# Performance work log

Hardware: AMD Instinct MI355X
Metric: run time of the kernel (lower is better)

Reference implementation:

```python
import jax, jax.numpy as jnp
import numpy as np

NEG_INF = -9e15
LEAKY_SLOPE = 0.2  # init alpha
N, IN_DIM, OUT_DIM = 8192, 512, 256


def setup_inputs() -> dict:
    key = jax.random.key(0)
    k1, k2, k3, k4, k5 = jax.random.split(key, 5)
    h = jax.random.normal(k1, (N, IN_DIM), dtype=jnp.float32)
    adj = jax.random.randint(k2, (N, N), 0, 2, dtype=jnp.int32)
    W = jax.random.normal(k3, (IN_DIM, OUT_DIM), dtype=jnp.float32) * 0.06
    a_left = jax.random.normal(k4, (OUT_DIM, 1), dtype=jnp.float32) * 0.1
    a_right = jax.random.normal(k5, (OUT_DIM, 1), dtype=jnp.float32) * 0.1
    return {"h": h, "adj": adj, "W": W, "a_left": a_left, "a_right": a_right}


def reference(h, adj, W, a_left, a_right):
    Wh = h @ W                                  # [N, out_dim]
    Wh1 = Wh @ a_left                           # [N, 1]
    Wh2 = Wh @ a_right                          # [N, 1]
    e = Wh1 + Wh2.T                             # [N, N] broadcast additive scores
    e = jnp.where(e > 0, e, LEAKY_SLOPE * e)    # LeakyReLU
    e = jnp.where(adj > 0, e, NEG_INF)          # adjacency mask
    attention = jax.nn.softmax(e, axis=1)       # row-wise softmax (dropout=0, eval)
    h_out = attention @ Wh                      # [N, out_dim]
    return jax.nn.elu(h_out)                    # activation=True
```

## Files before the change

### kernel.cpp

```cpp
#include <hip/hip_runtime.h>
#include <hip/hip_bf16.h>
#include <cstdint>
#include <cstddef>

typedef float  f32x4  __attribute__((ext_vector_type(4)));
typedef __bf16 bf16x8 __attribute__((ext_vector_type(8)));

#define LOG2E 1.4426950408889634f

static constexpr int GN   = 8192;
static constexpr int GIN  = 512;
static constexpr int GOUT = 256;

static __device__ __forceinline__ void gload_lds16(const void* g, void* lds){
  typedef uint32_t __attribute__((address_space(1)))* gp_t;
  typedef uint32_t __attribute__((address_space(3)))* lp_t;
  __builtin_amdgcn_global_load_lds((gp_t)(uintptr_t)g,
                                   (lp_t)(uint32_t)(uintptr_t)lds, 16, 0, 0);
}

__global__ __launch_bounds__(256) void k_pre1(const float* __restrict__ W,
                                              const float* __restrict__ al,
                                              const float* __restrict__ ar,
                                              const float* __restrict__ h,
                                              float* __restrict__ wal,
                                              float* __restrict__ war,
                                              __bf16* __restrict__ WT,
                                              __bf16* __restrict__ hb){
  __shared__ float T[64][65];
  const int bid = blockIdx.x, tid = threadIdx.x;
  if(bid < 128){
    const int k = bid*4 + (tid>>6), lane = tid & 63;
    float4 wv = ((const float4*)(W + (size_t)k*GOUT))[lane];
    float4 av = ((const float4*)al)[lane];
    float4 bv = ((const float4*)ar)[lane];
    float sl = wv.x*av.x + wv.y*av.y + wv.z*av.z + wv.w*av.w;
    float sr = wv.x*bv.x + wv.y*bv.y + wv.z*bv.z + wv.w*bv.w;
    #pragma unroll
    for(int o=32;o;o>>=1){ sl += __shfl_down(sl,o,64); sr += __shfl_down(sr,o,64); }
    if(lane==0){ wal[k] = sl*LOG2E; war[k] = sr*LOG2E; }
  } else if(bid < 160){
    const int tile = bid - 128;
    const int k0 = (tile>>2)*64, c0 = (tile&3)*64;
    const int r = tid>>2, cs = (tid&3)*16;
    #pragma unroll
    for(int j=0;j<4;j++){
      float4 v = *(const float4*)(W + (size_t)(k0+r)*GOUT + c0 + cs + 4*j);
      T[r][cs+4*j+0]=v.x; T[r][cs+4*j+1]=v.y; T[r][cs+4*j+2]=v.z; T[r][cs+4*j+3]=v.w;
    }
    __syncthreads();
    bf16x8 o1, o2;
    #pragma unroll
    for(int j=0;j<8;j++){ o1[j]=(__bf16)T[cs+j][r]; o2[j]=(__bf16)T[cs+8+j][r]; }
    __bf16* dst = WT + (size_t)(c0+r)*GIN + k0 + cs;
    *(bf16x8*)dst = o1;
    *(bf16x8*)(dst+8) = o2;
  } else {
    size_t i = ((size_t)(bid-160)*256 + tid)*8;
    float4 v0 = *(const float4*)(h+i);
    float4 v1 = *(const float4*)(h+i+4);
    bf16x8 o;
    o[0]=(__bf16)v0.x; o[1]=(__bf16)v0.y; o[2]=(__bf16)v0.z; o[3]=(__bf16)v0.w;
    o[4]=(__bf16)v1.x; o[5]=(__bf16)v1.y; o[6]=(__bf16)v1.z; o[7]=(__bf16)v1.w;
    *(bf16x8*)(hb+i) = o;
  }
}

__global__ __launch_bounds__(256) void k_pre2(const int* __restrict__ adj,
                                              unsigned int* __restrict__ pk,
                                              const __bf16* __restrict__ WT,
                                              const __bf16* __restrict__ hb,
                                              __bf16* __restrict__ WhbT,
                                              const float* __restrict__ h,
                                              const float* __restrict__ wal,
                                              const float* __restrict__ war,
                                              float* __restrict__ Wh1,
                                              float* __restrict__ Wh2){
  __shared__ __attribute__((aligned(16))) __bf16 As[2][64*64];
  __shared__ __attribute__((aligned(16))) __bf16 Bs[2][128*64];
  const int bid = blockIdx.x, tid = threadIdx.x;
  const int lane = tid & 63, w = tid >> 6;

  if(bid < 2048){
    const int Wv = bid*4 + w;
    const int jb = Wv & 127;
    const int g  = Wv >> 7;
    const size_t cb = (size_t)jb*64 + lane;
    const int idx = lane & 15;
    #pragma unroll 1
    for(int i=0;i<8;i++){
      const int r0 = (g*8 + i)*16;
      int a[16];
      #pragma unroll
      for(int r=0;r<16;r++) a[r] = adj[(size_t)(r0+r)*GN + cb];
      uint64_t b0 = __ballot(a[0]!=0),  b1 = __ballot(a[1]!=0);
      uint64_t b2 = __ballot(a[2]!=0),  b3 = __ballot(a[3]!=0);
      uint64_t b4 = __ballot(a[4]!=0),  b5 = __ballot(a[5]!=0);
      uint64_t b6 = __ballot(a[6]!=0),  b7 = __ballot(a[7]!=0);
      uint64_t b8 = __ballot(a[8]!=0),  b9 = __ballot(a[9]!=0);
      uint64_t bA = __ballot(a[10]!=0), bB = __ballot(a[11]!=0);
      uint64_t bC = __ballot(a[12]!=0), bD = __ballot(a[13]!=0);
      uint64_t bE = __ballot(a[14]!=0), bF = __ballot(a[15]!=0);
      uint64_t c0 = (idx&1)? b1:b0, c1 = (idx&1)? b3:b2;
      uint64_t c2 = (idx&1)? b5:b4, c3 = (idx&1)? b7:b6;
      uint64_t c4 = (idx&1)? b9:b8, c5 = (idx&1)? bB:bA;
      uint64_t c6 = (idx&1)? bD:bC, c7 = (idx&1)? bF:bE;
      uint64_t d0 = (idx&2)? c1:c0, d1 = (idx&2)? c3:c2;
      uint64_t d2 = (idx&2)? c5:c4, d3 = (idx&2)? c7:c6;
      uint64_t e0 = (idx&4)? d1:d0, e1 = (idx&4)? d3:d2;
      uint64_t v  = (idx&8)? e1:e0;
      unsigned int hword = (lane&16)? (unsigned int)(v>>32) : (unsigned int)v;
      if(lane < 32){
        pk[(size_t)(2*jb + (lane>>4))*GN + r0 + idx] = hword;
      }
    }
  } else if(bid < 2304){
    const int b2 = bid - 2048;
    const int mb = b2 >> 6, nb = b2 & 63;
    const int m0 = mb*64, n0 = nb*128;

    f32x4 acc[8];
    #pragma unroll
    for(int t=0;t<8;t++) acc[t] = (f32x4){0.f,0.f,0.f,0.f};

    const int lr = lane>>3;
    const int bs_sw = ((lane&7)*16) ^ (lr<<4);

    auto stage = [&](int it, int buf){
      const int k0b = it*128;
      #pragma unroll
      for(int s=0;s<6;s++){
        int u = w + s*4;
        const char* src; char* dst;
        if(u < 8){
          int r8 = u*8;
          src = (const char*)(WT + (size_t)(m0 + r8 + lr)*GIN);
          dst = (char*)&As[buf][0] + r8*128;
        } else {
          int r8 = (u-8)*8;
          src = (const char*)(hb + (size_t)(n0 + r8 + lr)*GIN);
          dst = (char*)&Bs[buf][0] + r8*128;
        }
        gload_lds16(src + k0b + bs_sw, dst);
      }
    };

    auto kstep = [&](int kk, int buf){
      const int ko = kk*64 + (lane>>4)*16;
      const int am = 16*w + (lane&15);
      bf16x8 af = *(const bf16x8*)((const char*)&As[buf][0] + am*128 + (ko ^ ((am&7)<<4)));
      #pragma unroll
      for(int t=0;t<8;t++){
        int n = 16*t + (lane&15);
        bf16x8 bf = *(const bf16x8*)((const char*)&Bs[buf][0] + n*128 + (ko ^ ((n&7)<<4)));
        acc[t] = __builtin_amdgcn_mfma_f32_16x16x32_bf16(af, bf, acc[t], 0, 0, 0);
      }
    };

    stage(0,0);
    asm volatile("s_waitcnt vmcnt(0)" ::: "memory");
    __builtin_amdgcn_s_barrier();
    for(int it=0; it<8; it++){
      int buf = it & 1;
      if(it < 7) stage(it+1, buf^1);
      kstep(0, buf);
      kstep(1, buf);
      asm volatile("s_waitcnt vmcnt(0)" ::: "memory");
      __builtin_amdgcn_s_barrier();
    }

    const int mrow = m0 + 16*w + 4*(lane>>4);
    const int nc0  = n0 + (lane&15);
    #pragma unroll
    for(int t=0;t<8;t++){
      #pragma unroll
      for(int r=0;r<4;r++){
        WhbT[(size_t)(mrow + r)*GN + nc0 + 16*t] = (__bf16)acc[t][r];
      }
    }
  } else {
    const int row = (bid-2304)*4 + w;
    const float4* hp = (const float4*)(h + (size_t)row*GIN);
    float4 v0 = hp[lane*2], v1 = hp[lane*2+1];
    float4 a0 = ((const float4*)wal)[lane*2], a1 = ((const float4*)wal)[lane*2+1];
    float4 b0 = ((const float4*)war)[lane*2], b1 = ((const float4*)war)[lane*2+1];
    float sl = v0.x*a0.x+v0.y*a0.y+v0.z*a0.z+v0.w*a0.w
             + v1.x*a1.x+v1.y*a1.y+v1.z*a1.z+v1.w*a1.w;
    float sr = v0.x*b0.x+v0.y*b0.y+v0.z*b0.z+v0.w*b0.w
             + v1.x*b1.x+v1.y*b1.y+v1.z*b1.z+v1.w*b1.w;
    #pragma unroll
    for(int of=32;of;of>>=1){ sl += __shfl_down(sl,of,64); sr += __shfl_down(sr,of,64); }
    if(lane==0){ Wh1[row]=sl; Wh2[row]=sr; }
  }
}

template<bool PART>
__global__ __launch_bounds__(256,2) void k_attn(const unsigned int* __restrict__ pk,
                                                const __bf16* __restrict__ WhbT,
                                                const float* __restrict__ Wh1s,
                                                const float* __restrict__ Wh2s,
                                                float* __restrict__ pv_out,
                                                float* __restrict__ s_out){
  __shared__ __attribute__((aligned(16))) char Vs[2][16384];
  __shared__ __attribute__((aligned(16))) unsigned int mkL[32*128];
  __shared__ __attribute__((aligned(16))) float wh2L[1024];
  const int tid = threadIdx.x, lane = tid & 63, w = tid >> 6;
  const int rg = blockIdx.x >> 3, chunk = blockIdx.x & 7;
  const int r0 = rg * 128;
  const int j0 = chunk * 1024;
  const int la = lane & 15, kg = lane >> 4, kg8 = kg << 3;

  const int jrow = tid >> 5, c4 = (tid & 31) * 4;
  uint4 mv0 = *(const uint4*)(pk + (size_t)(chunk*32 +  0 + jrow)*GN + r0 + c4);
  uint4 mv1 = *(const uint4*)(pk + (size_t)(chunk*32 +  8 + jrow)*GN + r0 + c4);
  uint4 mv2 = *(const uint4*)(pk + (size_t)(chunk*32 + 16 + jrow)*GN + r0 + c4);
  uint4 mv3 = *(const uint4*)(pk + (size_t)(chunk*32 + 24 + jrow)*GN + r0 + c4);
  float4 wv = *(const float4*)(Wh2s + j0 + tid*4);
  const float wh1_0 = Wh1s[r0 + 16*w + la];
  const float wh1_1 = Wh1s[r0 + 16*w + la + 64];

  const int l_log = (lane&7) ^ (lane>>3);
  const char* wbase = (const char*)WhbT
                    + (size_t)(64*w + 2*(lane>>3) + (l_log>>2))*(GN*2)
                    + (size_t)(l_log&3)*16;
  auto stage = [&](int it, int buf){
    const size_t colb = (size_t)(j0 + it*32)*2;
    char* dst = &Vs[buf][0] + w*4096 + lane*16;
    #pragma unroll
    for(int s=0;s<4;s++){
      gload_lds16(wbase + (size_t)(16*s)*(GN*2) + colb, dst + s*1024);
    }
  };

  stage(0, 0);

  *(uint4*)&mkL[( 0 + jrow)*128 + c4] = mv0;
  *(uint4*)&mkL[( 8 + jrow)*128 + c4] = mv1;
  *(uint4*)&mkL[(16 + jrow)*128 + c4] = mv2;
  *(uint4*)&mkL[(24 + jrow)*128 + c4] = mv3;
  *(float4*)&wh2L[tid*4] = wv;

  f32x4 acc0[16], acc1[16];
  #pragma unroll
  for(int t=0;t<16;t++){ acc0[t] = (f32x4){0.f,0.f,0.f,0.f}; acc1[t] = (f32x4){0.f,0.f,0.f,0.f}; }
  f32x4 accs0 = (f32x4){0.f,0.f,0.f,0.f};
  f32x4 accs1 = (f32x4){0.f,0.f,0.f,0.f};
  bf16x8 ones;
  #pragma unroll
  for(int j=0;j<8;j++) ones[j] = (__bf16)1.0f;

  __syncthreads();

  auto mkpa = [&](float wh1, unsigned m8, float4 w0, float4 w1) -> bf16x8 {
    bf16x8 pa;
    float y, p;
    y = wh1 + w0.x; y = fmaxf(y, 0.2f*y); p = exp2f(y); pa[0] = (__bf16)((m8    )&1 ? p : 0.f);
    y = wh1 + w0.y; y = fmaxf(y, 0.2f*y); p = exp2f(y); pa[1] = (__bf16)((m8>>1)&1 ? p : 0.f);
    y = wh1 + w0.z; y = fmaxf(y, 0.2f*y); p = exp2f(y); pa[2] = (__bf16)((m8>>2)&1 ? p : 0.f);
    y = wh1 + w0.w; y = fmaxf(y, 0.2f*y); p = exp2f(y); pa[3] = (__bf16)((m8>>3)&1 ? p : 0.f);
    y = wh1 + w1.x; y = fmaxf(y, 0.2f*y); p = exp2f(y); pa[4] = (__bf16)((m8>>4)&1 ? p : 0.f);
    y = wh1 + w1.y; y = fmaxf(y, 0.2f*y); p = exp2f(y); pa[5] = (__bf16)((m8>>5)&1 ? p : 0.f);
    y = wh1 + w1.z; y = fmaxf(y, 0.2f*y); p = exp2f(y); pa[6] = (__bf16)((m8>>6)&1 ? p : 0.f);
    y = wh1 + w1.w; y = fmaxf(y, 0.2f*y); p = exp2f(y); pa[7] = (__bf16)((m8>>7)&1 ? p : 0.f);
    return pa;
  };

  const int rd_off = (la>>1)*128 + (((((la&1)<<2) | kg) ^ (la>>1)) << 4);

  auto kstep = [&](int it, int buf){
    unsigned int m0 = mkL[it*128 + 16*w + la];
    unsigned int m1 = mkL[it*128 + 16*w + la + 64];
    const float* wp = &wh2L[it*32 + kg8];
    float4 w0 = *(const float4*)wp;
    float4 w1 = *(const float4*)(wp + 4);
    bf16x8 pa0 = mkpa(wh1_0, (m0 >> kg8) & 0xffu, w0, w1);
    bf16x8 pa1 = mkpa(wh1_1, (m1 >> kg8) & 0xffu, w0, w1);
    const char* vb = &Vs[buf][0] + rd_off;
    #pragma unroll
    for(int t=0;t<16;t++){
      bf16x8 bv = *(const bf16x8*)(vb + t*1024);
      acc0[t] = __builtin_amdgcn_mfma_f32_16x16x32_bf16(pa0, bv, acc0[t], 0, 0, 0);
      acc1[t] = __builtin_amdgcn_mfma_f32_16x16x32_bf16(pa1, bv, acc1[t], 0, 0, 0);
    }
    accs0 = __builtin_amdgcn_mfma_f32_16x16x32_bf16(pa0, ones, accs0, 0, 0, 0);
    accs1 = __builtin_amdgcn_mfma_f32_16x16x32_bf16(pa1, ones, accs1, 0, 0, 0);
  };

  for(int it=0; it<32; it++){
    const int buf = it & 1;
    if(it < 31) stage(it+1, buf^1);
    kstep(it, buf);
    asm volatile("s_waitcnt vmcnt(0)" ::: "memory");
    __builtin_amdgcn_s_barrier();
  }

  const int orow0 = r0 + 16*w + 4*kg;
  const int orow1 = orow0 + 64;
  const int ocol  = la;
  if constexpr (PART){
    float* pv = pv_out + (size_t)chunk*GN*GOUT;
    float* sp = s_out  + (size_t)chunk*GN;
    #pragma unroll
    for(int t=0;t<16;t++){
      #pragma unroll
      for(int r=0;r<4;r++){
        pv[(size_t)(orow0 + r)*GOUT + ocol + 16*t] = acc0[t][r];
        pv[(size_t)(orow1 + r)*GOUT + ocol + 16*t] = acc1[t][r];
      }
    }
    if(ocol == 0){
      #pragma unroll
      for(int r=0;r<4;r++){ sp[orow0 + r] = accs0[r]; sp[orow1 + r] = accs1[r]; }
    }
  } else {
    #pragma unroll
    for(int t=0;t<16;t++){
      #pragma unroll
      for(int r=0;r<4;r++){
        atomicAdd(pv_out + (size_t)(orow0 + r)*GOUT + ocol + 16*t, acc0[t][r]);
        atomicAdd(pv_out + (size_t)(orow1 + r)*GOUT + ocol + 16*t, acc1[t][r]);
      }
    }
    if(ocol == 0){
      #pragma unroll
      for(int r=0;r<4;r++){ atomicAdd(s_out + orow0 + r, accs0[r]); atomicAdd(s_out + orow1 + r, accs1[r]); }
    }
  }
}

static __device__ __forceinline__ float elu1(float x){
  return x > 0.f ? x : (exp2f(x*LOG2E) - 1.f);
}

__global__ void k_reduce(const float* __restrict__ accP, const float* __restrict__ accSp,
                         float* __restrict__ out){
  size_t i = ((size_t)blockIdx.x*256 + threadIdx.x)*4;
  int row = (int)(i >> 8);
  float S = 0.f;
  #pragma unroll
  for(int c=0;c<8;c++) S += accSp[(size_t)c*GN + row];
  float4 s = {0.f,0.f,0.f,0.f};
  #pragma unroll
  for(int c=0;c<8;c++){
    float4 v = *(const float4*)(accP + (size_t)c*GN*GOUT + i);
    s.x += v.x; s.y += v.y; s.z += v.z; s.w += v.w;
  }
  float inv = 1.0f / S;
  float4 o;
  o.x = elu1(s.x*inv); o.y = elu1(s.y*inv); o.z = elu1(s.z*inv); o.w = elu1(s.w*inv);
  *(float4*)(out + i) = o;
}

__global__ void k_norm(const float* __restrict__ accPV, const float* __restrict__ accS,
                       float* __restrict__ out){
  size_t i = ((size_t)blockIdx.x*256 + threadIdx.x)*4;
  int row = (int)(i >> 8);
  float inv = 1.0f / accS[row];
  float4 v = *(const float4*)(accPV + i);
  float4 o;
  o.x = elu1(v.x*inv); o.y = elu1(v.y*inv); o.z = elu1(v.z*inv); o.w = elu1(v.w*inv);
  *(float4*)(out + i) = o;
}

extern "C" void kernel_launch(void* const* d_in, const int* in_sizes, int n_in,
                              void* d_out, int out_size, void* d_ws, size_t ws_size,
                              hipStream_t stream){
  const float* h  = (const float*)d_in[0];
  const int*   adj= (const int*)  d_in[1];
  const float* W  = (const float*)d_in[2];
  const float* al = (const float*)d_in[3];
  const float* ar = (const float*)d_in[4];
  float* out = (float*)d_out;
  char* ws = (char*)d_ws;

  const size_t SZ_ACCP = (size_t)8*GN*GOUT*4;
  const size_t SZ_PK   = (size_t)256*GN*4;
  const size_t NEED_A  = SZ_ACCP + 4194304 + 32768 + 32768 + 262144 + SZ_PK;

  if(ws_size >= NEED_A){
    float*  accP  = (float*) (ws);
    __bf16* hb    = (__bf16*)(ws);
    __bf16* WT    = (__bf16*)(ws + 8388608);
    float*  wal   = (float*) (ws + 8650752);
    float*  war   = (float*) (ws + 8652800);
    __bf16* WhbT  = (__bf16*)(ws + SZ_ACCP);
    float*  Wh1   = (float*) (ws + SZ_ACCP + 4194304);
    float*  Wh2   = (float*) (ws + SZ_ACCP + 4227072);
    float*  accSp = (float*) (ws + SZ_ACCP + 4259840);
    unsigned int* pk = (unsigned int*)(ws + SZ_ACCP + 4521984);

    k_pre1<<<2208, 256, 0, stream>>>(W, al, ar, h, wal, war, WT, hb);
    k_pre2<<<4352, 256, 0, stream>>>(adj, pk, WT, hb, WhbT, h, wal, war, Wh1, Wh2);
    k_attn<true><<<512, 256, 0, stream>>>(pk, WhbT, Wh1, Wh2, accP, accSp);
    k_reduce<<<2048, 256, 0, stream>>>(accP, accSp, out);
  } else {
    float*  accPV = (float*) (ws);
    float*  accS  = (float*) (ws + 8388608);
    __bf16* hb    = (__bf16*)(ws + 8421376);
    __bf16* WT    = (__bf16*)(ws + 16809984);
    __bf16* WhbT  = (__bf16*)(ws + 17072128);
    float*  wal   = (float*) (ws + 21266432);
    float*  war   = (float*) (ws + 21268480);
    float*  Wh1   = (float*) (ws + 21270528);
    float*  Wh2   = (float*) (ws + 21303296);
    unsigned int* pk = (unsigned int*)(ws + 21336064);
    if(ws_size < 21336064 + SZ_PK) return;

    hipMemsetAsync(accPV, 0, 8388608 + 32768, stream);
    k_pre1<<<2208, 256, 0, stream>>>(W, al, ar, h, wal, war, WT, hb);
    k_pre2<<<4352, 256, 0, stream>>>(adj, pk, WT, hb, WhbT, h, wal, war, Wh1, Wh2);
    k_attn<false><<<512, 256, 0, stream>>>(pk, WhbT, Wh1, Wh2, accPV, accS);
    k_norm<<<2048, 256, 0, stream>>>(accPV, accS, out);
  }
}
```

Measured before the change: 141.5 us.

## Fuse adjacency bit-packing into attention kernel, drop packed-mask buffer

Result: no change. 143.3 us (+1.3%).

```diff
diff --git a/kernel.cpp b/kernel.cpp
--- a/kernel.cpp
+++ b/kernel.cpp
@@ -66,9 +66,7 @@
   }
 }
 
-__global__ __launch_bounds__(256) void k_pre2(const int* __restrict__ adj,
-                                              unsigned int* __restrict__ pk,
-                                              const __bf16* __restrict__ WT,
+__global__ __launch_bounds__(256) void k_pre2(const __bf16* __restrict__ WT,
                                               const __bf16* __restrict__ hb,
                                               __bf16* __restrict__ WhbT,
                                               const float* __restrict__ h,
@@ -81,18 +79,132 @@
   const int bid = blockIdx.x, tid = threadIdx.x;
   const int lane = tid & 63, w = tid >> 6;
 
-  if(bid < 2048){
-    const int Wv = bid*4 + w;
-    const int jb = Wv & 127;
-    const int g  = Wv >> 7;
-    const size_t cb = (size_t)jb*64 + lane;
+  if(bid < 256){
+    const int mb = bid >> 6, nb = bid & 63;
+    const int m0 = mb*64, n0 = nb*128;
+
+    f32x4 acc[8];
+    #pragma unroll
+    for(int t=0;t<8;t++) acc[t] = (f32x4){0.f,0.f,0.f,0.f};
+
+    const int lr = lane>>3;
+    const int bs_sw = ((lane&7)*16) ^ (lr<<4);
+
+    auto stage = [&](int it, int buf){
+      const int k0b = it*128;
+      #pragma unroll
+      for(int s=0;s<6;s++){
+        int u = w + s*4;
+        const char* src; char* dst;
+        if(u < 8){
+          int r8 = u*8;
+          src = (const char*)(WT + (size_t)(m0 + r8 + lr)*GIN);
+          dst = (char*)&As[buf][0] + r8*128;
+        } else {
+          int r8 = (u-8)*8;
+          src = (const char*)(hb + (size_t)(n0 + r8 + lr)*GIN);
+          dst = (char*)&Bs[buf][0] + r8*128;
+        }
+        gload_lds16(src + k0b + bs_sw, dst);
+      }
+    };
+
+    auto kstep = [&](int kk, int buf){
+      const int ko = kk*64 + (lane>>4)*16;
+      const int am = 16*w + (lane&15);
+      bf16x8 af = *(const bf16x8*)((const char*)&As[buf][0] + am*128 + (ko ^ ((am&7)<<4)));
+      #pragma unroll
+      for(int t=0;t<8;t++){
+        int n = 16*t + (lane&15);
+        bf16x8 bf = *(const bf16x8*)((const char*)&Bs[buf][0] + n*128 + (ko ^ ((n&7)<<4)));
+        acc[t] = __builtin_amdgcn_mfma_f32_16x16x32_bf16(af, bf, acc[t], 0, 0, 0);
+      }
+    };
+
+    stage(0,0);
+    asm volatile("s_waitcnt vmcnt(0)" ::: "memory");
+    __builtin_amdgcn_s_barrier();
+    for(int it=0; it<8; it++){
+      int buf = it & 1;
+      if(it < 7) stage(it+1, buf^1);
+      kstep(0, buf);
+      kstep(1, buf);
+      asm volatile("s_waitcnt vmcnt(0)" ::: "memory");
+      __builtin_amdgcn_s_barrier();
+    }
+
+    const int mrow = m0 + 16*w + 4*(lane>>4);
+    const int nc0  = n0 + (lane&15);
+    #pragma unroll
+    for(int t=0;t<8;t++){
+      #pragma unroll
+      for(int r=0;r<4;r++){
+        WhbT[(size_t)(mrow + r)*GN + nc0 + 16*t] = (__bf16)acc[t][r];
+      }
+    }
+  } else {
+    const int row = (bid-256)*4 + w;
+    const float4* hp = (const float4*)(h + (size_t)row*GIN);
+    float4 v0 = hp[lane*2], v1 = hp[lane*2+1];
+    float4 a0 = ((const float4*)wal)[lane*2], a1 = ((const float4*)wal)[lane*2+1];
+    float4 b0 = ((const float4*)war)[lane*2], b1 = ((const float4*)war)[lane*2+1];
+    float sl = v0.x*a0.x+v0.y*a0.y+v0.z*a0.z+v0.w*a0.w
+             + v1.x*a1.x+v1.y*a1.y+v1.z*a1.z+v1.w*a1.w;
+    float sr = v0.x*b0.x+v0.y*b0.y+v0.z*b0.z+v0.w*b0.w
+             + v1.x*b1.x+v1.y*b1.y+v1.z*b1.z+v1.w*b1.w;
+    #pragma unroll
+    for(int of=32;of;of>>=1){ sl += __shfl_down(sl,of,64); sr += __shfl_down(sr,of,64); }
+    if(lane==0){ Wh1[row]=sl; Wh2[row]=sr; }
+  }
+}
+
+template<bool PART>
+__global__ __launch_bounds__(256,2) void k_attn(const int* __restrict__ adj,
+                                                const __bf16* __restrict__ WhbT,
+                                                const float* __restrict__ Wh1s,
+                                                const float* __restrict__ Wh2s,
+                                                float* __restrict__ pv_out,
+                                                float* __restrict__ s_out){
+  __shared__ __attribute__((aligned(16))) char Vs[2][16384];
+  __shared__ __attribute__((aligned(16))) unsigned int mkL[32*128];
+  __shared__ __attribute__((aligned(16))) float wh2L[1024];
+  const int tid = threadIdx.x, lane = tid & 63, w = tid >> 6;
+  const int rg = blockIdx.x >> 3, chunk = blockIdx.x & 7;
+  const int r0 = rg * 128;
+  const int j0 = chunk * 1024;
+  const int la = lane & 15, kg = lane >> 4, kg8 = kg << 3;
+
+  float4 wv = *(const float4*)(Wh2s + j0 + tid*4);
+  const float wh1_0 = Wh1s[r0 + 16*w + la];
+  const float wh1_1 = Wh1s[r0 + 16*w + la + 64];
+
+  const int l_log = (lane&7) ^ (lane>>3);
+  const char* wbase = (const char*)WhbT
+                    + (size_t)(64*w + 2*(lane>>3) + (l_log>>2))*(GN*2)
+                    + (size_t)(l_log&3)*16;
+  auto stage = [&](int it, int buf){
+    const size_t colb = (size_t)(j0 + it*32)*2;
+    char* dst = &Vs[buf][0] + w*4096 + lane*16;
+    #pragma unroll
+    for(int s=0;s<4;s++){
+      gload_lds16(wbase + (size_t)(16*s)*(GN*2) + colb, dst + s*1024);
+    }
+  };
+
+  stage(0, 0);
+
+  {
+    const size_t abase = (size_t)(r0 + 32*w)*GN + j0 + lane;
     const int idx = lane & 15;
-    #pragma unroll 1
-    for(int i=0;i<8;i++){
-      const int r0 = (g*8 + i)*16;
-      int a[16];
-      #pragma unroll
-      for(int r=0;r<16;r++) a[r] = adj[(size_t)(r0+r)*GN + cb];
+    int aA[16], aB[16];
+    auto mload = [&](int s, int (&a)[16]){
+      const int g = s >> 4, jb = s & 15;
+      const size_t o = abase + (size_t)(16*g)*GN + jb*64;
+      #pragma unroll
+      for(int r=0;r<16;r++) a[r] = adj[o + (size_t)r*GN];
+    };
+    auto mpack = [&](int s, int (&a)[16]){
+      const int g = s >> 4, jb = s & 15;
       uint64_t b0 = __ballot(a[0]!=0),  b1 = __ballot(a[1]!=0);
       uint64_t b2 = __ballot(a[2]!=0),  b3 = __ballot(a[3]!=0);
       uint64_t b4 = __ballot(a[4]!=0),  b5 = __ballot(a[5]!=0);
@@ -111,133 +223,20 @@
       uint64_t v  = (idx&8)? e1:e0;
       unsigned int hword = (lane&16)? (unsigned int)(v>>32) : (unsigned int)v;
       if(lane < 32){
-        pk[(size_t)(2*jb + (lane>>4))*GN + r0 + idx] = hword;
-      }
-    }
-  } else if(bid < 2304){
-    const int b2 = bid - 2048;
-    const int mb = b2 >> 6, nb = b2 & 63;
-    const int m0 = mb*64, n0 = nb*128;
-
-    f32x4 acc[8];
-    #pragma unroll
-    for(int t=0;t<8;t++) acc[t] = (f32x4){0.f,0.f,0.f,0.f};
-
-    const int lr = lane>>3;
-    const int bs_sw = ((lane&7)*16) ^ (lr<<4);
-
-    auto stage = [&](int it, int buf){
-      const int k0b = it*128;
-      #pragma unroll
-      for(int s=0;s<6;s++){
-        int u = w + s*4;
-        const char* src; char* dst;
-        if(u < 8){
-          int r8 = u*8;
-          src = (const char*)(WT + (size_t)(m0 + r8 + lr)*GIN);
-          dst = (char*)&As[buf][0] + r8*128;
-        } else {
-          int r8 = (u-8)*8;
-          src = (const char*)(hb + (size_t)(n0 + r8 + lr)*GIN);
-          dst = (char*)&Bs[buf][0] + r8*128;
-        }
-        gload_lds16(src + k0b + bs_sw, dst);
+        mkL[(2*jb + (lane>>4))*128 + 32*w + 16*g + idx] = hword;
       }
     };
-
-    auto kstep = [&](int kk, int buf){
-      const int ko = kk*64 + (lane>>4)*16;
-      const int am = 16*w + (lane&15);
-      bf16x8 af = *(const bf16x8*)((const char*)&As[buf][0] + am*128 + (ko ^ ((am&7)<<4)));
-      #pragma unroll
-      for(int t=0;t<8;t++){
-        int n = 16*t + (lane&15);
-        bf16x8 bf = *(const bf16x8*)((const char*)&Bs[buf][0] + n*128 + (ko ^ ((n&7)<<4)));
-        acc[t] = __builtin_amdgcn_mfma_f32_16x16x32_bf16(af, bf, acc[t], 0, 0, 0);
-      }
-    };
-
-    stage(0,0);
-    asm volatile("s_waitcnt vmcnt(0)" ::: "memory");
-    __builtin_amdgcn_s_barrier();
-    for(int it=0; it<8; it++){
-      int buf = it & 1;
-      if(it < 7) stage(it+1, buf^1);
-      kstep(0, buf);
-      kstep(1, buf);
-      asm volatile("s_waitcnt vmcnt(0)" ::: "memory");
-      __builtin_amdgcn_s_barrier();
-    }
-
-    const int mrow = m0 + 16*w + 4*(lane>>4);
-    const int nc0  = n0 + (lane&15);
-    #pragma unroll
-    for(int t=0;t<8;t++){
-      #pragma unroll
-      for(int r=0;r<4;r++){
-        WhbT[(size_t)(mrow + r)*GN + nc0 + 16*t] = (__bf16)acc[t][r];
-      }
-    }
-  } else {
-    const int row = (bid-2304)*4 + w;
-    const float4* hp = (const float4*)(h + (size_t)row*GIN);
-    float4 v0 = hp[lane*2], v1 = hp[lane*2+1];
-    float4 a0 = ((const float4*)wal)[lane*2], a1 = ((const float4*)wal)[lane*2+1];
-    float4 b0 = ((const float4*)war)[lane*2], b1 = ((const float4*)war)[lane*2+1];
-    float sl = v0.x*a0.x+v0.y*a0.y+v0.z*a0.z+v0.w*a0.w
-             + v1.x*a1.x+v1.y*a1.y+v1.z*a1.z+v1.w*a1.w;
-    float sr = v0.x*b0.x+v0.y*b0.y+v0.z*b0.z+v0.w*b0.w
-             + v1.x*b1.x+v1.y*b1.y+v1.z*b1.z+v1.w*b1.w;
-    #pragma unroll
-    for(int of=32;of;of>>=1){ sl += __shfl_down(sl,of,64); sr += __shfl_down(sr,of,64); }
-    if(lane==0){ Wh1[row]=sl; Wh2[row]=sr; }
-  }
-}
-
-template<bool PART>
-__global__ __launch_bounds__(256,2) void k_attn(const unsigned int* __restrict__ pk,
-                                                const __bf16* __restrict__ WhbT,
-                                                const float* __restrict__ Wh1s,
-                                                const float* __restrict__ Wh2s,
-                                                float* __restrict__ pv_out,
-                                                float* __restrict__ s_out){
-  __shared__ __attribute__((aligned(16))) char Vs[2][16384];
-  __shared__ __attribute__((aligned(16))) unsigned int mkL[32*128];
-  __shared__ __attribute__((aligned(16))) float wh2L[1024];
-  const int tid = threadIdx.x, lane = tid & 63, w = tid >> 6;
-  const int rg = blockIdx.x >> 3, chunk = blockIdx.x & 7;
-  const int r0 = rg * 128;
-  const int j0 = chunk * 1024;
-  const int la = lane & 15, kg = lane >> 4, kg8 = kg << 3;
-
-  const int jrow = tid >> 5, c4 = (tid & 31) * 4;
-  uint4 mv0 = *(const uint4*)(pk + (size_t)(chunk*32 +  0 + jrow)*GN + r0 + c4);
-  uint4 mv1 = *(const uint4*)(pk + (size_t)(chunk*32 +  8 + jrow)*GN + r0 + c4);
-  uint4 mv2 = *(const uint4*)(pk + (size_t)(chunk*32 + 16 + jrow)*GN + r0 + c4);
-  uint4 mv3 = *(const uint4*)(pk + (size_t)(chunk*32 + 24 + jrow)*GN + r0 + c4);
-  float4 wv = *(const float4*)(Wh2s + j0 + tid*4);
-  const float wh1_0 = Wh1s[r0 + 16*w + la];
-  const float wh1_1 = Wh1s[r0 + 16*w + la + 64];
-
-  const int l_log = (lane&7) ^ (lane>>3);
-  const char* wbase = (const char*)WhbT
-                    + (size_t)(64*w + 2*(lane>>3) + (l_log>>2))*(GN*2)
-                    + (size_t)(l_log&3)*16;
-  auto stage = [&](int it, int buf){
-    const size_t colb = (size_t)(j0 + it*32)*2;
-    char* dst = &Vs[buf][0] + w*4096 + lane*16;
-    #pragma unroll
-    for(int s=0;s<4;s++){
-      gload_lds16(wbase + (size_t)(16*s)*(GN*2) + colb, dst + s*1024);
-    }
-  };
-
-  stage(0, 0);
-
-  *(uint4*)&mkL[( 0 + jrow)*128 + c4] = mv0;
-  *(uint4*)&mkL[( 8 + jrow)*128 + c4] = mv1;
-  *(uint4*)&mkL[(16 + jrow)*128 + c4] = mv2;
-  *(uint4*)&mkL[(24 + jrow)*128 + c4] = mv3;
+    mload(0, aA);
+    #pragma unroll 1
+    for(int sp=0; sp<16; ++sp){
+      const int s0 = 2*sp, s1 = s0+1;
+      mload(s1, aB);
+      mpack(s0, aA);
+      if(sp < 15) mload(s1+1, aA);
+      mpack(s1, aB);
+    }
+  }
+
   *(float4*)&wh2L[tid*4] = wv;
 
   f32x4 acc0[16], acc1[16];
@@ -374,8 +373,7 @@
   char* ws = (char*)d_ws;
 
   const size_t SZ_ACCP = (size_t)8*GN*GOUT*4;
-  const size_t SZ_PK   = (size_t)256*GN*4;
-  const size_t NEED_A  = SZ_ACCP + 4194304 + 32768 + 32768 + 262144 + SZ_PK;
+  const size_t NEED_A  = SZ_ACCP + 4194304 + 32768 + 32768 + 262144;
 
   if(ws_size >= NEED_A){
     float*  accP  = (float*) (ws);
@@ -387,11 +385,10 @@
     float*  Wh1   = (float*) (ws + SZ_ACCP + 4194304);
     float*  Wh2   = (float*) (ws + SZ_ACCP + 4227072);
     float*  accSp = (float*) (ws + SZ_ACCP + 4259840);
-    unsigned int* pk = (unsigned int*)(ws + SZ_ACCP + 4521984);
 
     k_pre1<<<2208, 256, 0, stream>>>(W, al, ar, h, wal, war, WT, hb);
-    k_pre2<<<4352, 256, 0, stream>>>(adj, pk, WT, hb, WhbT, h, wal, war, Wh1, Wh2);
-    k_attn<true><<<512, 256, 0, stream>>>(pk, WhbT, Wh1, Wh2, accP, accSp);
+    k_pre2<<<2304, 256, 0, stream>>>(WT, hb, WhbT, h, wal, war, Wh1, Wh2);
+    k_attn<true><<<512, 256, 0, stream>>>(adj, WhbT, Wh1, Wh2, accP, accSp);
     k_reduce<<<2048, 256, 0, stream>>>(accP, accSp, out);
   } else {
     float*  accPV = (float*) (ws);
@@ -403,13 +400,12 @@
     float*  war   = (float*) (ws + 21268480);
     float*  Wh1   = (float*) (ws + 21270528);
     float*  Wh2   = (float*) (ws + 21303296);
-    unsigned int* pk = (unsigned int*)(ws + 21336064);
-    if(ws_size < 21336064 + SZ_PK) return;
+    if(ws_size < 21336064) return;
 
     hipMemsetAsync(accPV, 0, 8388608 + 32768, stream);
     k_pre1<<<2208, 256, 0, stream>>>(W, al, ar, h, wal, war, WT, hb);
-    k_pre2<<<4352, 256, 0, stream>>>(adj, pk, WT, hb, WhbT, h, wal, war, Wh1, Wh2);
-    k_attn<false><<<512, 256, 0, stream>>>(pk, WhbT, Wh1, Wh2, accPV, accS);
+    k_pre2<<<2304, 256, 0, stream>>>(WT, hb, WhbT, h, wal, war, Wh1, Wh2);
+    k_attn<false><<<512, 256, 0, stream>>>(adj, WhbT, Wh1, Wh2, accPV, accS);
     k_norm<<<2048, 256, 0, stream>>>(accPV, accS, out);
   }
 }
```
